# Kernel optimization log

Hardware: AMD Instinct MI355X
Metric: run time of the kernel (lower is better)

## Reference

```python
import jax, jax.numpy as jnp
import numpy as np

N, E, G = 100000, 400000, 2000   # nodes, edges, graphs
IN, H = 48, 128                  # in_channels, hidden_channels (= out_channels)
L = 6                            # num GIN layers
EPS = 1e-5                       # BatchNorm eps
SLOPE = 0.01                     # leaky_relu negative slope


def setup_inputs() -> dict:
    key = jax.random.key(0)
    ks = jax.random.split(key, 12)
    x = jax.random.normal(ks[0], (N, IN), jnp.float32)
    edge_index = jax.random.randint(ks[1], (2, E), 0, N)
    edge_attr = jax.random.normal(ks[2], (E, 4), jnp.float32)  # ignored by GINConv
    # sorted graph-assignment vector; guarantee every graph has >=1 node
    batch = jnp.sort(jnp.concatenate([jnp.arange(G),
                                      jax.random.randint(ks[3], (N - G,), 0, G)]))
    s = 0.05
    W1a = jax.random.normal(ks[4], (IN, H), jnp.float32) * s        # layer-0 MLP lin1
    W1b = jax.random.normal(ks[5], (L - 1, H, H), jnp.float32) * s  # layers 1..5 MLP lin1
    b1 = jnp.zeros((L, H), jnp.float32)
    g1 = jnp.ones((L, H), jnp.float32)    # inner BN scale
    be1 = jnp.zeros((L, H), jnp.float32)  # inner BN bias
    W2 = jax.random.normal(ks[6], (L, H, H), jnp.float32) * s       # MLP lin2
    b2 = jnp.zeros((L, H), jnp.float32)
    gn = jnp.ones((L - 1, H), jnp.float32)    # outer BN scale (layers 0..4)
    bn_b = jnp.zeros((L - 1, H), jnp.float32) # outer BN bias
    fc_w = jax.random.normal(ks[7], (2 * H, 64), jnp.float32) * s
    fc_b = jnp.zeros((64,), jnp.float32)
    fc2_w = jax.random.normal(ks[8], (64, 3), jnp.float32) * s
    fc2_b = jnp.zeros((3,), jnp.float32)
    return dict(x=x, edge_attr=edge_attr, W1a=W1a, W1b=W1b, b1=b1, g1=g1, be1=be1,
                W2=W2, b2=b2, gn=gn, bn_b=bn_b, fc_w=fc_w, fc_b=fc_b,
                fc2_w=fc2_w, fc2_b=fc2_b, edge_index=edge_index, batch=batch,
                num_graphs=G)


def _bn(h, g, b):
    # training-mode BatchNorm1d over node dim (biased variance, as torch)
    m = jnp.mean(h, axis=0)
    v = jnp.mean((h - m) ** 2, axis=0)
    return g * (h - m) * jax.lax.rsqrt(v + EPS) + b


def _lrelu(h):
    return jnp.where(h >= 0, h, SLOPE * h)


def reference(x, edge_attr, W1a, W1b, b1, g1, be1, W2, b2, gn, bn_b,
              fc_w, fc_b, fc2_w, fc2_b, edge_index, batch, num_graphs):
    del edge_attr  # GINConv does not use edge attributes
    src, dst = edge_index[0], edge_index[1]
    n = x.shape[0]
    h = x
    for l in range(L):
        # GINConv: (1 + eps) * x + sum_{j in N(i)} x_j, eps = 0
        agg = jax.ops.segment_sum(h[src], dst, num_segments=n)
        z = h + agg
        W1 = W1a if l == 0 else W1b[l - 1]
        # MLP([in, H, H]) with inner BatchNorm + leaky_relu, plain last linear
        z = _lrelu(_bn(z @ W1 + b1[l], g1[l], be1[l])) @ W2[l] + b2[l]
        if l < L - 1:  # outer norm + act, skipped on last layer
            z = _lrelu(_bn(z, gn[l], bn_b[l]))
        h = z
    # dual global pooling over ragged per-graph segments
    cnt = jax.ops.segment_sum(jnp.ones((n, 1), h.dtype), batch, num_segments=num_graphs)
    p1 = jax.ops.segment_sum(h, batch, num_segments=num_graphs) / jnp.maximum(cnt, 1.0)
    p2 = jax.ops.segment_max(h, batch, num_segments=num_graphs)
    emb = jnp.concatenate([p1, p2], axis=1)            # [G, 256]
    out = _lrelu(emb @ fc_w + fc_b) @ fc2_w + fc2_b    # [G, 3]
    return out, emb
```

## Files before the change

### kernel.cpp

```cpp
#include <hip/hip_runtime.h>
#include <stdint.h>

#define N_NODES 100000
#define N_EDGES 400000
#define N_GRAPHS 2000
#define C_IN 48
#define HD 128
#define NLAYERS 6
#define BN_EPS 1e-5f
#define NSLOPE 0.01f
#define SB 391
#define NREP 8
#define DBINS 33

typedef uint16_t u16;
typedef uint32_t u32;
typedef short bf16x8 __attribute__((ext_vector_type(8)));
typedef float f32x4 __attribute__((ext_vector_type(4)));

__device__ __forceinline__ float bf2f_lo(u32 v) { return __uint_as_float(v << 16); }
__device__ __forceinline__ float bf2f_hi(u32 v) { return __uint_as_float(v & 0xffff0000u); }
__device__ __forceinline__ float bf2f(u16 h) { return __uint_as_float(((u32)h) << 16); }
__device__ __forceinline__ u16 f2bf(float f) {
    u32 u = __float_as_uint(f);
    u32 r = (u + 0x7fffu + ((u >> 16) & 1u)) >> 16;
    return (u16)r;
}
__device__ __forceinline__ u32 pack2(float a, float b) {
    return (u32)f2bf(a) | ((u32)f2bf(b) << 16);
}
__device__ __forceinline__ float lrelu(float v) { return v >= 0.f ? v : v * NSLOPE; }

__device__ __forceinline__ void acc_bn(float* a, const uint4 v, const float* cA, const float* cB) {
    const u32 w[4] = {v.x, v.y, v.z, v.w};
    #pragma unroll
    for (int p = 0; p < 4; ++p) {
        a[2 * p]     += lrelu(cA[2 * p] * bf2f_lo(w[p]) + cB[2 * p]);
        a[2 * p + 1] += lrelu(cA[2 * p + 1] * bf2f_hi(w[p]) + cB[2 * p + 1]);
    }
}
__device__ __forceinline__ void acc_bf16row(float* a, const uint4 v) {
    const u32 w[4] = {v.x, v.y, v.z, v.w};
    #pragma unroll
    for (int p = 0; p < 4; ++p) {
        a[2 * p]     += bf2f_lo(w[p]);
        a[2 * p + 1] += bf2f_hi(w[p]);
    }
}
__device__ __forceinline__ void acc_f32row(float* a, const float* p) {
    const float4 u0 = reinterpret_cast<const float4*>(p)[0];
    const float4 u1 = reinterpret_cast<const float4*>(p)[1];
    a[0] += u0.x; a[1] += u0.y; a[2] += u0.z; a[3] += u0.w;
    a[4] += u1.x; a[5] += u1.y; a[6] += u1.z; a[7] += u1.w;
}
__device__ __forceinline__ void ld_xrow(float* a, const void* xv, int md, int idx, int seg) {
    if (md) acc_f32row(a, (const float*)xv + (size_t)idx * C_IN + seg * 8);
    else    acc_bf16row(a, *reinterpret_cast<const uint4*>((const u16*)xv + (size_t)idx * C_IN + seg * 8));
}

__global__ __launch_bounds__(256) void detect_kernel(const u16* __restrict__ x, int* __restrict__ mode) {
    __shared__ int flag;
    if (threadIdx.x == 0) flag = 0;
    __syncthreads();
    int local = 0;
    for (int i = threadIdx.x; i < 16384; i += 256) {
        float a = fabsf(bf2f(x[i]));
        if (!(a < 1e4f)) local = 1;
    }
    if (local) flag = 1;
    __syncthreads();
    if (threadIdx.x == 0) mode[0] = flag;
}

__global__ __launch_bounds__(256) void hist_kernel(const int* __restrict__ dst, int* __restrict__ cnt) {
    int e = blockIdx.x * 256 + threadIdx.x;
    if (e < N_EDGES) atomicAdd(&cnt[dst[e]], 1);
}

__global__ __launch_bounds__(256) void scan1_kernel(const int* __restrict__ cnt, int* __restrict__ bsum) {
    __shared__ int s[256];
    const int t = threadIdx.x;
    const int i = blockIdx.x * 256 + t;
    s[t] = (i < N_NODES) ? cnt[i] : 0;
    __syncthreads();
    for (int d = 128; d > 0; d >>= 1) {
        if (t < d) s[t] += s[t + d];
        __syncthreads();
    }
    if (t == 0) bsum[blockIdx.x] = s[0];
}

__global__ __launch_bounds__(512) void scan2_kernel(int* __restrict__ bsum, int* __restrict__ row_ptr) {
    __shared__ int s[SB];
    const int t = threadIdx.x;
    if (t < SB) s[t] = bsum[t];
    __syncthreads();
    if (t == 0) {
        int run = 0;
        for (int b = 0; b < SB; ++b) { int v = s[b]; s[b] = run; run += v; }
        row_ptr[0] = 0;
    }
    __syncthreads();
    if (t < SB) bsum[t] = s[t];
}

__global__ __launch_bounds__(256) void scan3_kernel(const int* __restrict__ cnt, const int* __restrict__ bsum,
                                                    int* __restrict__ row_ptr) {
    __shared__ int s[256];
    const int t = threadIdx.x;
    const int i = blockIdx.x * 256 + t;
    s[t] = (i < N_NODES) ? cnt[i] : 0;
    __syncthreads();
    if (t == 0) {
        int run = bsum[blockIdx.x];
        for (int j = 0; j < 256; ++j) { run += s[j]; s[j] = run; }
    }
    __syncthreads();
    if (i < N_NODES) row_ptr[i + 1] = s[t];
}

__global__ __launch_bounds__(256) void fill_kernel(const int* __restrict__ src, const int* __restrict__ dst,
                                                   const int* __restrict__ pos,
                                                   int* __restrict__ cursor, int* __restrict__ col_idx) {
    int e = blockIdx.x * 256 + threadIdx.x;
    if (e < N_EDGES) {
        int d = dst[e];
        int slot = atomicAdd(&cursor[d], 1);
        col_idx[slot] = pos[src[e]];
    }
}

__global__ __launch_bounds__(256) void deg_hist_kernel(const int* __restrict__ row_ptr, int* __restrict__ dbins) {
    __shared__ int h[DBINS];
    const int tid = threadIdx.x;
    if (tid < DBINS) h[tid] = 0;
    __syncthreads();
    const int i = blockIdx.x * 256 + tid;
    if (i < N_NODES) atomicAdd(&h[min(row_ptr[i + 1] - row_ptr[i], 32)], 1);
    __syncthreads();
    if (tid < DBINS && h[tid]) atomicAdd(&dbins[tid], h[tid]);
}

__global__ __launch_bounds__(64) void deg_scan_kernel(int* __restrict__ dbins) {
    if (threadIdx.x == 0) {
        int run = 0;
        for (int b = DBINS - 1; b >= 0; --b) { int v = dbins[b]; dbins[b] = run; run += v; }
    }
}

__global__ __launch_bounds__(256) void deg_scatter_kernel(const int* __restrict__ row_ptr, int* __restrict__ dbins,
                                                          int* __restrict__ perm) {
    __shared__ int cnt[DBINS];
    __shared__ int base[DBINS];
    const int tid = threadIdx.x;
    const int i = blockIdx.x * 256 + tid;
    if (tid < DBINS) cnt[tid] = 0;
    __syncthreads();
    int d = 0, local = 0;
    const bool act = i < N_NODES;
    if (act) {
        d = min(row_ptr[i + 1] - row_ptr[i], 32);
        local = atomicAdd(&cnt[d], 1);
    }
    __syncthreads();
    if (tid < DBINS) base[tid] = cnt[tid] ? atomicAdd(&dbins[tid], cnt[tid]) : 0;
    __syncthreads();
    if (act) perm[base[d] + local] = i;
}

__global__ __launch_bounds__(256) void inv_kernel(const int* __restrict__ perm, int* __restrict__ pos) {
    const int i = blockIdx.x * 256 + threadIdx.x;
    if (i < N_NODES) pos[perm[i]] = i;
}

__global__ __launch_bounds__(256) void pack_w_kernel(const void* __restrict__ W1a, const void* __restrict__ W1b,
                                                     const void* __restrict__ W2, const int* __restrict__ mode,
                                                     u16* __restrict__ wpack) {
    const int t = blockIdx.x * 256 + threadIdx.x;
    if (t >= 24576) return;
    const int mat = t >> 11;
    const int r = t & 2047;
    const int l = r & 63;
    const int f = r >> 6;
    const int kb = f >> 3, nt = f & 7;
    const int k0 = kb * 32 + (l >> 4) * 8;
    const int n = nt * 16 + (l & 15);
    const int md = *mode;
    u16 vals[8];
    #pragma unroll
    for (int j = 0; j < 8; ++j) {
        const int k = k0 + j;
        float v;
        if (mat == 0) {
            v = (k < C_IN) ? (md ? ((const float*)W1a)[k * HD + n] : bf2f(((const u16*)W1a)[k * HD + n])) : 0.f;
        } else if (mat < 6) {
            const size_t o = (size_t)(mat - 1) * HD * HD + (size_t)k * HD + n;
            v = md ? ((const float*)W1b)[o] : bf2f(((const u16*)W1b)[o]);
        } else {
            const size_t o = (size_t)(mat - 6) * HD * HD + (size_t)k * HD + n;
            v = md ? ((const float*)W2)[o] : bf2f(((const u16*)W2)[o]);
        }
        vals[j] = f2bf(v);
    }
    uint4 o;
    o.x = (u32)vals[0] | ((u32)vals[1] << 16);
    o.y = (u32)vals[2] | ((u32)vals[3] << 16);
    o.z = (u32)vals[4] | ((u32)vals[5] << 16);
    o.w = (u32)vals[6] | ((u32)vals[7] << 16);
    *reinterpret_cast<uint4*>(wpack + (size_t)t * 8) = o;
}

__global__ __launch_bounds__(256) void pack_b_kernel(const void* __restrict__ b1, const void* __restrict__ b2,
                                                     const int* __restrict__ mode, float* __restrict__ biasf) {
    const int i = blockIdx.x * 256 + threadIdx.x;
    if (i >= 12 * HD) return;
    const int mat = i >> 7, c = i & 127;
    const int md = *mode;
    float v;
    if (mat < 6) v = md ? ((const float*)b1)[mat * HD + c] : bf2f(((const u16*)b1)[mat * HD + c]);
    else         v = md ? ((const float*)b2)[(mat - 6) * HD + c] : bf2f(((const u16*)b2)[(mat - 6) * HD + c]);
    biasf[i] = v;
}

__device__ __forceinline__ void coef_to_lds(float* coefs, const float* __restrict__ instats,
                                            const void* __restrict__ gammav, const void* __restrict__ betav,
                                            size_t gelem, int md, int tid) {
    if (tid < 128) {
        float sm = 0.f, sq = 0.f;
        #pragma unroll
        for (int rep = 0; rep < NREP; ++rep) {
            sm += instats[rep * 256 + tid];
            sq += instats[rep * 256 + 128 + tid];
        }
        const float inv_n = 1.0f / (float)N_NODES;
        const float mean = sm * inv_n;
        const float var = fmaxf(sq * inv_n - mean * mean, 0.f);
        const float rs = rsqrtf(var + BN_EPS);
        const float g  = md ? ((const float*)gammav)[gelem + tid] : bf2f(((const u16*)gammav)[gelem + tid]);
        const float be = md ? ((const float*)betav)[gelem + tid]  : bf2f(((const u16*)betav)[gelem + tid]);
        const float A = g * rs;
        coefs[tid] = A;
        coefs[128 + tid] = be - A * mean;
    }
}

template <int TRANS, int STATS>
__global__ __launch_bounds__(256) void gemm_mfma(const u16* A, const u16* __restrict__ wp,
                                                 const float* __restrict__ biasf,
                                                 const float* __restrict__ instats,
                                                 const void* __restrict__ gammav, const void* __restrict__ betav,
                                                 size_t gelem, const int* __restrict__ mode,
                                                 u16* out, float* __restrict__ stats) {
    __shared__ u16 Asm[32][136];
    __shared__ float sred[2][128];
    __shared__ float sqred[2][128];
    __shared__ float coefs[256];
    const int tid = threadIdx.x;
    const int m0 = blockIdx.x * 32;
    const int rrow = tid >> 4;
    const int seg = tid & 15;

    if (TRANS) {
        coef_to_lds(coefs, instats, gammav, betav, gelem, *mode, tid);
        __syncthreads();
    }

    {
        float cA[8], cB[8];
        if (TRANS) {
            #pragma unroll
            for (int j = 0; j < 8; ++j) {
                cA[j] = coefs[seg * 8 + j];
                cB[j] = coefs[128 + seg * 8 + j];
            }
        }
        uint4 v[2];
        #pragma unroll
        for (int i = 0; i < 2; ++i) {
            const int gm = m0 + i * 16 + rrow;
            if (gm < N_NODES) v[i] = *reinterpret_cast<const uint4*>(A + (size_t)gm * HD + seg * 8);
            else { v[i].x = 0; v[i].y = 0; v[i].z = 0; v[i].w = 0; }
        }
        #pragma unroll
        for (int i = 0; i < 2; ++i) {
            uint4 o = v[i];
            if (TRANS) {
                u32 w[4] = {o.x, o.y, o.z, o.w};
                #pragma unroll
                for (int p = 0; p < 4; ++p) {
                    const float lo = lrelu(cA[2 * p] * bf2f_lo(w[p]) + cB[2 * p]);
                    const float hi = lrelu(cA[2 * p + 1] * bf2f_hi(w[p]) + cB[2 * p + 1]);
                    w[p] = pack2(lo, hi);
                }
                o.x = w[0]; o.y = w[1]; o.z = w[2]; o.w = w[3];
            }
            *reinterpret_cast<uint4*>(&Asm[i * 16 + rrow][seg * 8]) = o;
        }
    }
    __syncthreads();

    const int wave = tid >> 6, lane = tid & 63;
    const int quad = lane >> 4, lx = lane & 15;
    const int rowhalf = wave & 1;
    const int colhalf = wave >> 1;
    const int wrow = rowhalf * 16;
    f32x4 acc[4] = {};
    #pragma unroll
    for (int kb = 0; kb < 4; ++kb) {
        bf16x8 bfr[4];
        #pragma unroll
        for (int nt = 0; nt < 4; ++nt)
            bfr[nt] = *reinterpret_cast<const bf16x8*>(wp + (((size_t)(kb * 8 + colhalf * 4 + nt) * 64 + lane) << 3));
        const bf16x8 af = *reinterpret_cast<const bf16x8*>(&Asm[wrow + lx][kb * 32 + quad * 8]);
        #pragma unroll
        for (int nt = 0; nt < 4; ++nt)
            acc[nt] = __builtin_amdgcn_mfma_f32_16x16x32_bf16(af, bfr[nt], acc[nt], 0, 0, 0);
    }

    const int mrow0 = m0 + wrow;
    #pragma unroll
    for (int nt = 0; nt < 4; ++nt) {
        const int n = colhalf * 64 + nt * 16 + lx;
        const float bj = biasf[n];
        float s = 0.f, q = 0.f;
        #pragma unroll
        for (int r = 0; r < 4; ++r) {
            const int m = mrow0 + quad * 4 + r;
            if (m < N_NODES) {
                const float v = acc[nt][r] + bj;
                out[(size_t)m * HD + n] = f2bf(v);
                if (STATS) { s += v; q += v * v; }
            }
        }
        if (STATS) {
            s += __shfl_xor(s, 16); s += __shfl_xor(s, 32);
            q += __shfl_xor(q, 16); q += __shfl_xor(q, 32);
            if (quad == 0) { sred[rowhalf][n] = s; sqred[rowhalf][n] = q; }
        }
    }
    if (STATS) {
        __syncthreads();
        float* sdst = stats + (size_t)(blockIdx.x & (NREP - 1)) * 256;
        if (tid < 128) {
            atomicAdd(&sdst[tid], sred[0][tid] + sred[1][tid]);
        } else if (tid < 256) {
            const int c2 = tid - 128;
            atomicAdd(&sdst[128 + c2], sqred[0][c2] + sqred[1][c2]);
        }
    }
}

__global__ __launch_bounds__(256) void gemm_gather(const u16* __restrict__ U, const int* __restrict__ row_ptr,
                                                   const int* __restrict__ col2, const int* __restrict__ perm,
                                                   const u16* __restrict__ wp,
                                                   const float* __restrict__ biasf,
                                                   const float* __restrict__ instats,
                                                   const void* __restrict__ gammav, const void* __restrict__ betav,
                                                   size_t gelem, const int* __restrict__ mode,
                                                   u16* __restrict__ out, float* __restrict__ stats) {
    __shared__ u16 Asm[32][136];
    __shared__ float sred[2][128];
    __shared__ float sqred[2][128];
    __shared__ float coefs[256];
    const int tid = threadIdx.x;
    const int m0 = blockIdx.x * 32;
    const int rrow = tid >> 4;
    const int seg = tid & 15;

    coef_to_lds(coefs, instats, gammav, betav, gelem, *mode, tid);
    __syncthreads();

    {
        float cA[8], cB[8];
        #pragma unroll
        for (int j = 0; j < 8; ++j) {
            cA[j] = coefs[seg * 8 + j];
            cB[j] = coefs[128 + seg * 8 + j];
        }
        const int lm0 = m0 + rrow;
        const int lm1 = m0 + 16 + rrow;
        const int gm0 = perm[lm0];
        const int gm1 = perm[lm1];
        float a0[8], a1[8];
        #pragma unroll
        for (int j = 0; j < 8; ++j) { a0[j] = 0.f; a1[j] = 0.f; }
        const uint4 v0 = *reinterpret_cast<const uint4*>(U + (size_t)lm0 * HD + seg * 8);
        const uint4 v1 = *reinterpret_cast<const uint4*>(U + (size_t)lm1 * HD + seg * 8);
        acc_bn(a0, v0, cA, cB);
        acc_bn(a1, v1, cA, cB);
        const int s0 = row_ptr[gm0], d0 = row_ptr[gm0 + 1] - s0;
        const int s1 = row_ptr[gm1], d1 = row_ptr[gm1 + 1] - s1;
        const int dm = max(d0, d1);
        for (int t = 0; t < dm; t += 2) {
            const bool p00 = t < d0, p01 = (t + 1) < d0;
            const bool p10 = t < d1, p11 = (t + 1) < d1;
            int i00 = 0, i01 = 0, i10 = 0, i11 = 0;
            if (p00) i00 = col2[s0 + t];
            if (p01) i01 = col2[s0 + t + 1];
            if (p10) i10 = col2[s1 + t];
            if (p11) i11 = col2[s1 + t + 1];
            uint4 r00{}, r01{}, r10{}, r11{};
            if (p00) r00 = *reinterpret_cast<const uint4*>(U + (size_t)i00 * HD + seg * 8);
            if (p01) r01 = *reinterpret_cast<const uint4*>(U + (size_t)i01 * HD + seg * 8);
            if (p10) r10 = *reinterpret_cast<const uint4*>(U + (size_t)i10 * HD + seg * 8);
            if (p11) r11 = *reinterpret_cast<const uint4*>(U + (size_t)i11 * HD + seg * 8);
            if (p00) acc_bn(a0, r00, cA, cB);
            if (p01) acc_bn(a0, r01, cA, cB);
            if (p10) acc_bn(a1, r10, cA, cB);
            if (p11) acc_bn(a1, r11, cA, cB);
        }
        uint4 o0, o1;
        o0.x = pack2(a0[0], a0[1]); o0.y = pack2(a0[2], a0[3]);
        o0.z = pack2(a0[4], a0[5]); o0.w = pack2(a0[6], a0[7]);
        o1.x = pack2(a1[0], a1[1]); o1.y = pack2(a1[2], a1[3]);
        o1.z = pack2(a1[4], a1[5]); o1.w = pack2(a1[6], a1[7]);
        *reinterpret_cast<uint4*>(&Asm[rrow][seg * 8]) = o0;
        *reinterpret_cast<uint4*>(&Asm[16 + rrow][seg * 8]) = o1;
    }
    __syncthreads();

    const int wave = tid >> 6, lane = tid & 63;
    const int quad = lane >> 4, lx = lane & 15;
    const int rowhalf = wave & 1;
    const int colhalf = wave >> 1;
    const int wrow = rowhalf * 16;
    f32x4 acc[4] = {};
    #pragma unroll
    for (int kb = 0; kb < 4; ++kb) {
        bf16x8 bfr[4];
        #pragma unroll
        for (int nt = 0; nt < 4; ++nt)
            bfr[nt] = *reinterpret_cast<const bf16x8*>(wp + (((size_t)(kb * 8 + colhalf * 4 + nt) * 64 + lane) << 3));
        const bf16x8 af = *reinterpret_cast<const bf16x8*>(&Asm[wrow + lx][kb * 32 + quad * 8]);
        #pragma unroll
        for (int nt = 0; nt < 4; ++nt)
            acc[nt] = __builtin_amdgcn_mfma_f32_16x16x32_bf16(af, bfr[nt], acc[nt], 0, 0, 0);
    }

    const int mrow0 = m0 + wrow;
    #pragma unroll
    for (int nt = 0; nt < 4; ++nt) {
        const int n = colhalf * 64 + nt * 16 + lx;
        const float bj = biasf[n];
        float s = 0.f, q = 0.f;
        #pragma unroll
        for (int r = 0; r < 4; ++r) {
            const int m = mrow0 + quad * 4 + r;
            const float v = acc[nt][r] + bj;
            out[(size_t)m * HD + n] = f2bf(v);
            s += v; q += v * v;
        }
        s += __shfl_xor(s, 16); s += __shfl_xor(s, 32);
        q += __shfl_xor(q, 16); q += __shfl_xor(q, 32);
        if (quad == 0) { sred[rowhalf][n] = s; sqred[rowhalf][n] = q; }
    }
    __syncthreads();
    float* sdst = stats + (size_t)(blockIdx.x & (NREP - 1)) * 256;
    if (tid < 128) {
        atomicAdd(&sdst[tid], sred[0][tid] + sred[1][tid]);
    } else if (tid < 256) {
        const int c2 = tid - 128;
        atomicAdd(&sdst[128 + c2], sqred[0][c2] + sqred[1][c2]);
    }
}

__global__ __launch_bounds__(256) void gemm_gather0(const void* __restrict__ xv, const int* __restrict__ row_ptr,
                                                    const int* __restrict__ col2, const int* __restrict__ perm,
                                                    const u16* __restrict__ wp,
                                                    const float* __restrict__ biasf, const int* __restrict__ mode,
                                                    u16* __restrict__ out, float* __restrict__ stats) {
    __shared__ u16 Asm[32][136];
    __shared__ float sred[2][128];
    __shared__ float sqred[2][128];
    const int tid = threadIdx.x;
    const int m0 = blockIdx.x * 32;
    const int rrow = tid >> 4;
    const int seg = tid & 15;
    const int md = *mode;
    const bool act = seg < 6;

    {
        const int lm0 = m0 + rrow;
        const int lm1 = m0 + 16 + rrow;
        const int gm0 = perm[lm0];
        const int gm1 = perm[lm1];
        float a0[8], a1[8];
        #pragma unroll
        for (int j = 0; j < 8; ++j) { a0[j] = 0.f; a1[j] = 0.f; }
        const int s0 = row_ptr[gm0], d0 = row_ptr[gm0 + 1] - s0;
        const int s1 = row_ptr[gm1], d1 = row_ptr[gm1 + 1] - s1;
        if (act) {
            ld_xrow(a0, xv, md, gm0, seg);
            ld_xrow(a1, xv, md, gm1, seg);
            const int dm = max(d0, d1);
            for (int t = 0; t < dm; t += 2) {
                const bool p00 = t < d0, p01 = (t + 1) < d0;
                const bool p10 = t < d1, p11 = (t + 1) < d1;
                int i00 = 0, i01 = 0, i10 = 0, i11 = 0;
                if (p00) i00 = perm[col2[s0 + t]];
                if (p01) i01 = perm[col2[s0 + t + 1]];
                if (p10) i10 = perm[col2[s1 + t]];
                if (p11) i11 = perm[col2[s1 + t + 1]];
                if (p00) ld_xrow(a0, xv, md, i00, seg);
                if (p01) ld_xrow(a0, xv, md, i01, seg);
                if (p10) ld_xrow(a1, xv, md, i10, seg);
                if (p11) ld_xrow(a1, xv, md, i11, seg);
            }
        }
        uint4 o0, o1;
        o0.x = pack2(a0[0], a0[1]); o0.y = pack2(a0[2], a0[3]);
        o0.z = pack2(a0[4], a0[5]); o0.w = pack2(a0[6], a0[7]);
        o1.x = pack2(a1[0], a1[1]); o1.y = pack2(a1[2], a1[3]);
        o1.z = pack2(a1[4], a1[5]); o1.w = pack2(a1[6], a1[7]);
        *reinterpret_cast<uint4*>(&Asm[rrow][seg * 8]) = o0;
        *reinterpret_cast<uint4*>(&Asm[16 + rrow][seg * 8]) = o1;
    }
    __syncthreads();

    const int wave = tid >> 6, lane = tid & 63;
    const int quad = lane >> 4, lx = lane & 15;
    const int rowhalf = wave & 1;
    const int colhalf = wave >> 1;
    const int wrow = rowhalf * 16;
    f32x4 acc[4] = {};
    #pragma unroll
    for (int kb = 0; kb < 4; ++kb) {
        bf16x8 bfr[4];
        #pragma unroll
        for (int nt = 0; nt < 4; ++nt)
            bfr[nt] = *reinterpret_cast<const bf16x8*>(wp + (((size_t)(kb * 8 + colhalf * 4 + nt) * 64 + lane) << 3));
        const bf16x8 af = *reinterpret_cast<const bf16x8*>(&Asm[wrow + lx][kb * 32 + quad * 8]);
        #pragma unroll
        for (int nt = 0; nt < 4; ++nt)
            acc[nt] = __builtin_amdgcn_mfma_f32_16x16x32_bf16(af, bfr[nt], acc[nt], 0, 0, 0);
    }

    const int mrow0 = m0 + wrow;
    #pragma unroll
    for (int nt = 0; nt < 4; ++nt) {
        const int n = colhalf * 64 + nt * 16 + lx;
        const float bj = biasf[n];
        float s = 0.f, q = 0.f;
        #pragma unroll
        for (int r = 0; r < 4; ++r) {
            const int m = mrow0 + quad * 4 + r;
            const float v = acc[nt][r] + bj;
            out[(size_t)m * HD + n] = f2bf(v);
            s += v; q += v * v;
        }
        s += __shfl_xor(s, 16); s += __shfl_xor(s, 32);
        q += __shfl_xor(q, 16); q += __shfl_xor(q, 32);
        if (quad == 0) { sred[rowhalf][n] = s; sqred[rowhalf][n] = q; }
    }
    __syncthreads();
    float* sdst = stats + (size_t)(blockIdx.x & (NREP - 1)) * 256;
    if (tid < 128) {
        atomicAdd(&sdst[tid], sred[0][tid] + sred[1][tid]);
    } else if (tid < 256) {
        const int c2 = tid - 128;
        atomicAdd(&sdst[128 + c2], sqred[0][c2] + sqred[1][c2]);
    }
}

__global__ __launch_bounds__(256) void pool_kernel(const u16* __restrict__ hf, const int* __restrict__ batch,
                                                   const int* __restrict__ pos,
                                                   const int* __restrict__ mode, float* __restrict__ emb,
                                                   void* __restrict__ outv) {
    const int wave = threadIdx.x >> 6, lane = threadIdx.x & 63;
    const int g = blockIdx.x * 4 + wave;
    if (g >= N_GRAPHS) return;
    const int md = *mode;
    const int quad = lane >> 4, c = lane & 15;
    int lo = 0, hi = N_NODES;
    while (lo < hi) { int m = (lo + hi) >> 1; if (batch[m] < g) lo = m + 1; else hi = m; }
    const int s = lo;
    hi = N_NODES;
    while (lo < hi) { int m = (lo + hi) >> 1; if (batch[m] < g + 1) lo = m + 1; else hi = m; }
    const int e = lo;
    const int cnt = e - s;
    float sum[8], mx[8];
    #pragma unroll
    for (int j = 0; j < 8; ++j) { sum[j] = 0.f; mx[j] = -INFINITY; }
    for (int n = s + quad; n < e; n += 4) {
        const int p = pos[n];
        const uint4 v = *reinterpret_cast<const uint4*>(hf + (size_t)p * HD + c * 8);
        const u32 w[4] = {v.x, v.y, v.z, v.w};
        #pragma unroll
        for (int pp = 0; pp < 4; ++pp) {
            const float f0 = bf2f_lo(w[pp]), f1 = bf2f_hi(w[pp]);
            sum[2 * pp] += f0; sum[2 * pp + 1] += f1;
            mx[2 * pp] = fmaxf(mx[2 * pp], f0); mx[2 * pp + 1] = fmaxf(mx[2 * pp + 1], f1);
        }
    }
    #pragma unroll
    for (int j = 0; j < 8; ++j) {
        sum[j] += __shfl_xor(sum[j], 16); sum[j] += __shfl_xor(sum[j], 32);
        mx[j] = fmaxf(mx[j], __shfl_xor(mx[j], 16));
        mx[j] = fmaxf(mx[j], __shfl_xor(mx[j], 32));
    }
    if (quad == 0) {
        const float invc = 1.0f / (float)max(cnt, 1);
        const size_t base = (size_t)N_GRAPHS * 3 + (size_t)g * 256;
        #pragma unroll
        for (int j = 0; j < 8; ++j) {
            const float mean = sum[j] * invc;
            const float m2 = (cnt == 0) ? 0.f : mx[j];
            const int col = c * 8 + j;
            emb[(size_t)g * 256 + col] = mean;
            emb[(size_t)g * 256 + 128 + col] = m2;
            if (md) {
                ((float*)outv)[base + col] = mean;
                ((float*)outv)[base + 128 + col] = m2;
            } else {
                ((u16*)outv)[base + col] = f2bf(mean);
                ((u16*)outv)[base + 128 + col] = f2bf(m2);
            }
        }
    }
}

__global__ __launch_bounds__(64) void final_kernel(const float* __restrict__ emb, const void* __restrict__ fcwv,
                                                   const void* __restrict__ fcbv, const void* __restrict__ fc2wv,
                                                   const void* __restrict__ fc2bv, const int* __restrict__ mode,
                                                   void* __restrict__ outv) {
    __shared__ float es[256];
    __shared__ float hs[64];
    const int g = blockIdx.x, t = threadIdx.x;
    const int md = *mode;
    reinterpret_cast<float4*>(es)[t] = reinterpret_cast<const float4*>(emb + (size_t)g * 256)[t];
    __syncthreads();
    float acc = md ? ((const float*)fcbv)[t] : bf2f(((const u16*)fcbv)[t]);
    if (md) {
        const float* w = (const float*)fcwv;
        #pragma unroll 8
        for (int k = 0; k < 256; ++k) acc += es[k] * w[k * 64 + t];
    } else {
        const u16* w = (const u16*)fcwv;
        #pragma unroll 8
        for (int k = 0; k < 256; ++k) acc += es[k] * bf2f(w[k * 64 + t]);
    }
    hs[t] = lrelu(acc);
    __syncthreads();
    if (t < 3) {
        float o = md ? ((const float*)fc2bv)[t] : bf2f(((const u16*)fc2bv)[t]);
        if (md) {
            const float* w = (const float*)fc2wv;
            #pragma unroll 8
            for (int j = 0; j < 64; ++j) o += hs[j] * w[j * 3 + t];
            ((float*)outv)[(size_t)g * 3 + t] = o;
        } else {
            const u16* w = (const u16*)fc2wv;
            #pragma unroll 8
            for (int j = 0; j < 64; ++j) o += hs[j] * bf2f(w[j * 3 + t]);
            ((u16*)outv)[(size_t)g * 3 + t] = f2bf(o);
        }
    }
}

static inline size_t align256(size_t x) { return (x + 255) & ~(size_t)255; }

extern "C" void kernel_launch(void* const* d_in, const int* in_sizes, int n_in,
                              void* d_out, int out_size, void* d_ws, size_t ws_size,
                              hipStream_t stream) {
    (void)in_sizes; (void)n_in; (void)out_size; (void)ws_size;
    const void* x    = d_in[0];
    const void* W1a  = d_in[2];
    const void* W1b  = d_in[3];
    const void* b1   = d_in[4];
    const void* g1   = d_in[5];
    const void* be1  = d_in[6];
    const void* W2   = d_in[7];
    const void* b2   = d_in[8];
    const void* gn   = d_in[9];
    const void* bnb  = d_in[10];
    const void* fcw  = d_in[11];
    const void* fcb  = d_in[12];
    const void* fc2w = d_in[13];
    const void* fc2b = d_in[14];
    const int* ei    = (const int*)d_in[15];
    const int* batch = (const int*)d_in[16];

    char* p = (char*)d_ws;
    size_t off = 0;
    u16* zb = (u16*)(p + off); off += align256((size_t)N_NODES * HD * 2);
    u16* hb = (u16*)(p + off); off += align256((size_t)N_NODES * HD * 2);
    u16* wpack = (u16*)(p + off); off += align256((size_t)12 * HD * HD * 2);
    float* biasf = (float*)(p + off); off += align256((size_t)12 * HD * 4);
    float* emb = (float*)(p + off); off += align256((size_t)N_GRAPHS * 256 * 4);
    int* row_ptr = (int*)(p + off); off += align256((size_t)(N_NODES + 1) * 4);
    int* cursor = (int*)(p + off); off += align256((size_t)N_NODES * 4);
    int* col_idx = (int*)(p + off); off += align256((size_t)N_EDGES * 4);
    int* bsum = (int*)(p + off); off += align256((size_t)SB * 4);
    float* statsAll = (float*)(p + off); off += align256((size_t)12 * NREP * 256 * 4);
    int* perm = (int*)(p + off); off += align256((size_t)N_NODES * 4);
    int* pos = (int*)(p + off); off += align256((size_t)N_NODES * 4);
    int* dbins = (int*)(p + off); off += align256((size_t)64 * 4);
    int* mode = (int*)(p + off); off += align256(4);

    const int EB = (N_EDGES + 255) / 256;
    const int GB32 = N_NODES / 32;

    detect_kernel<<<1, 256, 0, stream>>>((const u16*)x, mode);

    hipMemsetAsync(cursor, 0, (size_t)N_NODES * 4, stream);
    hipMemsetAsync(statsAll, 0, (size_t)12 * NREP * 256 * 4, stream);
    hipMemsetAsync(dbins, 0, (size_t)DBINS * 4, stream);
    hist_kernel<<<EB, 256, 0, stream>>>(ei + N_EDGES, cursor);
    scan1_kernel<<<SB, 256, 0, stream>>>(cursor, bsum);
    scan2_kernel<<<1, 512, 0, stream>>>(bsum, row_ptr);
    scan3_kernel<<<SB, 256, 0, stream>>>(cursor, bsum, row_ptr);
    deg_hist_kernel<<<SB, 256, 0, stream>>>(row_ptr, dbins);
    deg_scan_kernel<<<1, 64, 0, stream>>>(dbins);
    deg_scatter_kernel<<<SB, 256, 0, stream>>>(row_ptr, dbins, perm);
    inv_kernel<<<SB, 256, 0, stream>>>(perm, pos);
    hipMemcpyAsync(cursor, row_ptr, (size_t)N_NODES * 4, hipMemcpyDeviceToDevice, stream);
    fill_kernel<<<EB, 256, 0, stream>>>(ei, ei + N_EDGES, pos, cursor, col_idx);
    pack_w_kernel<<<96, 256, 0, stream>>>(W1a, W1b, W2, mode, wpack);
    pack_b_kernel<<<6, 256, 0, stream>>>(b1, b2, mode, biasf);

    u16* cur = zb;
    u16* oth = hb;
    for (int l = 0; l < NLAYERS; ++l) {
        float* statsA = statsAll + (size_t)l * NREP * 256;
        float* statsB = statsAll + (size_t)(6 + l) * NREP * 256;
        float* statsBprev = statsAll + (size_t)(6 + l - 1) * NREP * 256;
        if (l == 0) {
            gemm_gather0<<<GB32, 256, 0, stream>>>(x, row_ptr, col_idx, perm, wpack,
                                                   biasf, mode, cur, statsA);
        } else {
            gemm_gather<<<GB32, 256, 0, stream>>>(cur, row_ptr, col_idx, perm,
                                                  wpack + (size_t)l * HD * HD,
                                                  biasf + (size_t)l * HD, statsBprev, gn, bnb,
                                                  (size_t)(l - 1) * HD, mode, oth, statsA);
            u16* t = cur; cur = oth; oth = t;
        }
        if (l < NLAYERS - 1) {
            gemm_mfma<1, 1><<<GB32, 256, 0, stream>>>(cur, wpack + (size_t)(6 + l) * HD * HD,
                                                      biasf + (size_t)(6 + l) * HD, statsA, g1, be1,
                                                      (size_t)l * HD, mode, cur, statsB);
        } else {
            gemm_mfma<1, 0><<<GB32, 256, 0, stream>>>(cur, wpack + (size_t)(6 + l) * HD * HD,
                                                      biasf + (size_t)(6 + l) * HD, statsA, g1, be1,
                                                      (size_t)l * HD, mode, cur, nullptr);
        }
    }

    pool_kernel<<<(N_GRAPHS + 3) / 4, 256, 0, stream>>>(cur, batch, pos, mode, emb, d_out);
    final_kernel<<<N_GRAPHS, 64, 0, stream>>>(emb, fcw, fcb, fc2w, fc2b, mode, d_out);
}
```

Baseline: 494.7 us.

## Unroll gathers by four, parallelize block scan, store raw source indices

The neighbor-gather loops in both gather GEMM kernels are unrolled from two to four neighbors per step, so more independent row loads are in flight. Layer 0 now reads a second column array holding raw source ids, which removes the perm indirection per edge at the cost of writing another 400K-int array. The serial single-thread scan in scan2 becomes a parallel Hillis-Steele scan. Row-bound checks in the GEMM are dropped (N is divisible by 32), and the shared epilogue is factored into a helper. The wider unroll raises register pressure.

```diff
diff --git a/kernel.cpp b/kernel.cpp
--- a/kernel.cpp
+++ b/kernel.cpp
@@ -91,17 +91,18 @@
 }
 
 __global__ __launch_bounds__(512) void scan2_kernel(int* __restrict__ bsum, int* __restrict__ row_ptr) {
-    __shared__ int s[SB];
+    __shared__ int s[512];
     const int t = threadIdx.x;
-    if (t < SB) s[t] = bsum[t];
-    __syncthreads();
-    if (t == 0) {
-        int run = 0;
-        for (int b = 0; b < SB; ++b) { int v = s[b]; s[b] = run; run += v; }
-        row_ptr[0] = 0;
-    }
-    __syncthreads();
-    if (t < SB) bsum[t] = s[t];
+    s[t] = (t < SB) ? bsum[t] : 0;
+    __syncthreads();
+    for (int d = 1; d < 512; d <<= 1) {
+        const int v = (t >= d) ? s[t - d] : 0;
+        __syncthreads();
+        s[t] += v;
+        __syncthreads();
+    }
+    if (t < SB) bsum[t] = (t == 0) ? 0 : s[t - 1];
+    if (t == 0) row_ptr[0] = 0;
 }
 
 __global__ __launch_bounds__(256) void scan3_kernel(const int* __restrict__ cnt, const int* __restrict__ bsum,
@@ -121,12 +122,15 @@
 
 __global__ __launch_bounds__(256) void fill_kernel(const int* __restrict__ src, const int* __restrict__ dst,
                                                    const int* __restrict__ pos,
-                                                   int* __restrict__ cursor, int* __restrict__ col_idx) {
+                                                   int* __restrict__ cursor, int* __restrict__ col_idx,
+                                                   int* __restrict__ col0_idx) {
     int e = blockIdx.x * 256 + threadIdx.x;
     if (e < N_EDGES) {
         int d = dst[e];
         int slot = atomicAdd(&cursor[d], 1);
-        col_idx[slot] = pos[src[e]];
+        const int sv = src[e];
+        col_idx[slot] = pos[sv];
+        col0_idx[slot] = sv;
     }
 }
 
@@ -244,6 +248,55 @@
     }
 }
 
+__device__ __forceinline__ void mfma_epilogue32(const u16 (*Asm)[136], const u16* __restrict__ wp,
+                                                const float* __restrict__ biasf,
+                                                float sred[2][128], float sqred[2][128],
+                                                int m0, int tid, int bidx,
+                                                u16* __restrict__ out, float* __restrict__ stats) {
+    const int wave = tid >> 6, lane = tid & 63;
+    const int quad = lane >> 4, lx = lane & 15;
+    const int rowhalf = wave & 1;
+    const int colhalf = wave >> 1;
+    const int wrow = rowhalf * 16;
+    f32x4 acc[4] = {};
+    #pragma unroll
+    for (int kb = 0; kb < 4; ++kb) {
+        bf16x8 bfr[4];
+        #pragma unroll
+        for (int nt = 0; nt < 4; ++nt)
+            bfr[nt] = *reinterpret_cast<const bf16x8*>(wp + (((size_t)(kb * 8 + colhalf * 4 + nt) * 64 + lane) << 3));
+        const bf16x8 af = *reinterpret_cast<const bf16x8*>(&Asm[wrow + lx][kb * 32 + quad * 8]);
+        #pragma unroll
+        for (int nt = 0; nt < 4; ++nt)
+            acc[nt] = __builtin_amdgcn_mfma_f32_16x16x32_bf16(af, bfr[nt], acc[nt], 0, 0, 0);
+    }
+    const int mrow0 = m0 + wrow;
+    #pragma unroll
+    for (int nt = 0; nt < 4; ++nt) {
+        const int n = colhalf * 64 + nt * 16 + lx;
+        const float bj = biasf[n];
+        float s = 0.f, q = 0.f;
+        #pragma unroll
+        for (int r = 0; r < 4; ++r) {
+            const int m = mrow0 + quad * 4 + r;
+            const float v = acc[nt][r] + bj;
+            out[(size_t)m * HD + n] = f2bf(v);
+            s += v; q += v * v;
+        }
+        s += __shfl_xor(s, 16); s += __shfl_xor(s, 32);
+        q += __shfl_xor(q, 16); q += __shfl_xor(q, 32);
+        if (quad == 0) { sred[rowhalf][n] = s; sqred[rowhalf][n] = q; }
+    }
+    __syncthreads();
+    float* sdst = stats + (size_t)(bidx & (NREP - 1)) * 256;
+    if (tid < 128) {
+        atomicAdd(&sdst[tid], sred[0][tid] + sred[1][tid]);
+    } else {
+        const int c2 = tid - 128;
+        atomicAdd(&sdst[128 + c2], sqred[0][c2] + sqred[1][c2]);
+    }
+}
+
 template <int TRANS, int STATS>
 __global__ __launch_bounds__(256) void gemm_mfma(const u16* A, const u16* __restrict__ wp,
                                                  const float* __restrict__ biasf,
@@ -278,8 +331,7 @@
         #pragma unroll
         for (int i = 0; i < 2; ++i) {
             const int gm = m0 + i * 16 + rrow;
-            if (gm < N_NODES) v[i] = *reinterpret_cast<const uint4*>(A + (size_t)gm * HD + seg * 8);
-            else { v[i].x = 0; v[i].y = 0; v[i].z = 0; v[i].w = 0; }
+            v[i] = *reinterpret_cast<const uint4*>(A + (size_t)gm * HD + seg * 8);
         }
         #pragma unroll
         for (int i = 0; i < 2; ++i) {
@@ -299,53 +351,36 @@
     }
     __syncthreads();
 
-    const int wave = tid >> 6, lane = tid & 63;
-    const int quad = lane >> 4, lx = lane & 15;
-    const int rowhalf = wave & 1;
-    const int colhalf = wave >> 1;
-    const int wrow = rowhalf * 16;
-    f32x4 acc[4] = {};
-    #pragma unroll
-    for (int kb = 0; kb < 4; ++kb) {
-        bf16x8 bfr[4];
-        #pragma unroll
-        for (int nt = 0; nt < 4; ++nt)
-            bfr[nt] = *reinterpret_cast<const bf16x8*>(wp + (((size_t)(kb * 8 + colhalf * 4 + nt) * 64 + lane) << 3));
-        const bf16x8 af = *reinterpret_cast<const bf16x8*>(&Asm[wrow + lx][kb * 32 + quad * 8]);
-        #pragma unroll
-        for (int nt = 0; nt < 4; ++nt)
-            acc[nt] = __builtin_amdgcn_mfma_f32_16x16x32_bf16(af, bfr[nt], acc[nt], 0, 0, 0);
-    }
-
-    const int mrow0 = m0 + wrow;
-    #pragma unroll
-    for (int nt = 0; nt < 4; ++nt) {
-        const int n = colhalf * 64 + nt * 16 + lx;
-        const float bj = biasf[n];
-        float s = 0.f, q = 0.f;
-        #pragma unroll
-        for (int r = 0; r < 4; ++r) {
-            const int m = mrow0 + quad * 4 + r;
-            if (m < N_NODES) {
-                const float v = acc[nt][r] + bj;
-                out[(size_t)m * HD + n] = f2bf(v);
-                if (STATS) { s += v; q += v * v; }
+    if (STATS) {
+        mfma_epilogue32(Asm, wp, biasf, sred, sqred, m0, tid, blockIdx.x, out, stats);
+    } else {
+        const int wave = tid >> 6, lane = tid & 63;
+        const int quad = lane >> 4, lx = lane & 15;
+        const int rowhalf = wave & 1;
+        const int colhalf = wave >> 1;
+        const int wrow = rowhalf * 16;
+        f32x4 acc[4] = {};
+        #pragma unroll
+        for (int kb = 0; kb < 4; ++kb) {
+            bf16x8 bfr[4];
+            #pragma unroll
+            for (int nt = 0; nt < 4; ++nt)
+                bfr[nt] = *reinterpret_cast<const bf16x8*>(wp + (((size_t)(kb * 8 + colhalf * 4 + nt) * 64 + lane) << 3));
+            const bf16x8 af = *reinterpret_cast<const bf16x8*>(&Asm[wrow + lx][kb * 32 + quad * 8]);
+            #pragma unroll
+            for (int nt = 0; nt < 4; ++nt)
+                acc[nt] = __builtin_amdgcn_mfma_f32_16x16x32_bf16(af, bfr[nt], acc[nt], 0, 0, 0);
+        }
+        const int mrow0 = m0 + wrow;
+        #pragma unroll
+        for (int nt = 0; nt < 4; ++nt) {
+            const int n = colhalf * 64 + nt * 16 + lx;
+            const float bj = biasf[n];
+            #pragma unroll
+            for (int r = 0; r < 4; ++r) {
+                const int m = mrow0 + quad * 4 + r;
+                out[(size_t)m * HD + n] = f2bf(acc[nt][r] + bj);
             }
-        }
-        if (STATS) {
-            s += __shfl_xor(s, 16); s += __shfl_xor(s, 32);
-            q += __shfl_xor(q, 16); q += __shfl_xor(q, 32);
-            if (quad == 0) { sred[rowhalf][n] = s; sqred[rowhalf][n] = q; }
-        }
-    }
-    if (STATS) {
-        __syncthreads();
-        float* sdst = stats + (size_t)(blockIdx.x & (NREP - 1)) * 256;
-        if (tid < 128) {
-            atomicAdd(&sdst[tid], sred[0][tid] + sred[1][tid]);
-        } else if (tid < 256) {
-            const int c2 = tid - 128;
-            atomicAdd(&sdst[128 + c2], sqred[0][c2] + sqred[1][c2]);
         }
     }
 }
@@ -391,23 +426,36 @@
         const int s0 = row_ptr[gm0], d0 = row_ptr[gm0 + 1] - s0;
         const int s1 = row_ptr[gm1], d1 = row_ptr[gm1 + 1] - s1;
         const int dm = max(d0, d1);
-        for (int t = 0; t < dm; t += 2) {
-            const bool p00 = t < d0, p01 = (t + 1) < d0;
-            const bool p10 = t < d1, p11 = (t + 1) < d1;
-            int i00 = 0, i01 = 0, i10 = 0, i11 = 0;
+        for (int t = 0; t < dm; t += 4) {
+            const bool p00 = t < d0, p01 = (t + 1) < d0, p02 = (t + 2) < d0, p03 = (t + 3) < d0;
+            const bool p10 = t < d1, p11 = (t + 1) < d1, p12 = (t + 2) < d1, p13 = (t + 3) < d1;
+            int i00 = 0, i01 = 0, i02 = 0, i03 = 0;
+            int i10 = 0, i11 = 0, i12 = 0, i13 = 0;
             if (p00) i00 = col2[s0 + t];
             if (p01) i01 = col2[s0 + t + 1];
+            if (p02) i02 = col2[s0 + t + 2];
+            if (p03) i03 = col2[s0 + t + 3];
             if (p10) i10 = col2[s1 + t];
             if (p11) i11 = col2[s1 + t + 1];
-            uint4 r00{}, r01{}, r10{}, r11{};
+            if (p12) i12 = col2[s1 + t + 2];
+            if (p13) i13 = col2[s1 + t + 3];
+            uint4 r00{}, r01{}, r02{}, r03{}, r10{}, r11{}, r12{}, r13{};
             if (p00) r00 = *reinterpret_cast<const uint4*>(U + (size_t)i00 * HD + seg * 8);
             if (p01) r01 = *reinterpret_cast<const uint4*>(U + (size_t)i01 * HD + seg * 8);
+            if (p02) r02 = *reinterpret_cast<const uint4*>(U + (size_t)i02 * HD + seg * 8);
+            if (p03) r03 = *reinterpret_cast<const uint4*>(U + (size_t)i03 * HD + seg * 8);
             if (p10) r10 = *reinterpret_cast<const uint4*>(U + (size_t)i10 * HD + seg * 8);
             if (p11) r11 = *reinterpret_cast<const uint4*>(U + (size_t)i11 * HD + seg * 8);
+            if (p12) r12 = *reinterpret_cast<const uint4*>(U + (size_t)i12 * HD + seg * 8);
+            if (p13) r13 = *reinterpret_cast<const uint4*>(U + (size_t)i13 * HD + seg * 8);
             if (p00) acc_bn(a0, r00, cA, cB);
             if (p01) acc_bn(a0, r01, cA, cB);
+            if (p02) acc_bn(a0, r02, cA, cB);
+            if (p03) acc_bn(a0, r03, cA, cB);
             if (p10) acc_bn(a1, r10, cA, cB);
             if (p11) acc_bn(a1, r11, cA, cB);
+            if (p12) acc_bn(a1, r12, cA, cB);
+            if (p13) acc_bn(a1, r13, cA, cB);
         }
         uint4 o0, o1;
         o0.x = pack2(a0[0], a0[1]); o0.y = pack2(a0[2], a0[3]);
@@ -419,53 +467,11 @@
     }
     __syncthreads();
 
-    const int wave = tid >> 6, lane = tid & 63;
-    const int quad = lane >> 4, lx = lane & 15;
-    const int rowhalf = wave & 1;
-    const int colhalf = wave >> 1;
-    const int wrow = rowhalf * 16;
-    f32x4 acc[4] = {};
-    #pragma unroll
-    for (int kb = 0; kb < 4; ++kb) {
-        bf16x8 bfr[4];
-        #pragma unroll
-        for (int nt = 0; nt < 4; ++nt)
-            bfr[nt] = *reinterpret_cast<const bf16x8*>(wp + (((size_t)(kb * 8 + colhalf * 4 + nt) * 64 + lane) << 3));
-        const bf16x8 af = *reinterpret_cast<const bf16x8*>(&Asm[wrow + lx][kb * 32 + quad * 8]);
-        #pragma unroll
-        for (int nt = 0; nt < 4; ++nt)
-            acc[nt] = __builtin_amdgcn_mfma_f32_16x16x32_bf16(af, bfr[nt], acc[nt], 0, 0, 0);
-    }
-
-    const int mrow0 = m0 + wrow;
-    #pragma unroll
-    for (int nt = 0; nt < 4; ++nt) {
-        const int n = colhalf * 64 + nt * 16 + lx;
-        const float bj = biasf[n];
-        float s = 0.f, q = 0.f;
-        #pragma unroll
-        for (int r = 0; r < 4; ++r) {
-            const int m = mrow0 + quad * 4 + r;
-            const float v = acc[nt][r] + bj;
-            out[(size_t)m * HD + n] = f2bf(v);
-            s += v; q += v * v;
-        }
-        s += __shfl_xor(s, 16); s += __shfl_xor(s, 32);
-        q += __shfl_xor(q, 16); q += __shfl_xor(q, 32);
-        if (quad == 0) { sred[rowhalf][n] = s; sqred[rowhalf][n] = q; }
-    }
-    __syncthreads();
-    float* sdst = stats + (size_t)(blockIdx.x & (NREP - 1)) * 256;
-    if (tid < 128) {
-        atomicAdd(&sdst[tid], sred[0][tid] + sred[1][tid]);
-    } else if (tid < 256) {
-        const int c2 = tid - 128;
-        atomicAdd(&sdst[128 + c2], sqred[0][c2] + sqred[1][c2]);
-    }
+    mfma_epilogue32(Asm, wp, biasf, sred, sqred, m0, tid, blockIdx.x, out, stats);
 }
 
 __global__ __launch_bounds__(256) void gemm_gather0(const void* __restrict__ xv, const int* __restrict__ row_ptr,
-                                                    const int* __restrict__ col2, const int* __restrict__ perm,
+                                                    const int* __restrict__ col0, const int* __restrict__ perm,
                                                     const u16* __restrict__ wp,
                                                     const float* __restrict__ biasf, const int* __restrict__ mode,
                                                     u16* __restrict__ out, float* __restrict__ stats) {
@@ -493,18 +499,27 @@
             ld_xrow(a0, xv, md, gm0, seg);
             ld_xrow(a1, xv, md, gm1, seg);
             const int dm = max(d0, d1);
-            for (int t = 0; t < dm; t += 2) {
-                const bool p00 = t < d0, p01 = (t + 1) < d0;
-                const bool p10 = t < d1, p11 = (t + 1) < d1;
-                int i00 = 0, i01 = 0, i10 = 0, i11 = 0;
-                if (p00) i00 = perm[col2[s0 + t]];
-                if (p01) i01 = perm[col2[s0 + t + 1]];
-                if (p10) i10 = perm[col2[s1 + t]];
-                if (p11) i11 = perm[col2[s1 + t + 1]];
+            for (int t = 0; t < dm; t += 4) {
+                const bool p00 = t < d0, p01 = (t + 1) < d0, p02 = (t + 2) < d0, p03 = (t + 3) < d0;
+                const bool p10 = t < d1, p11 = (t + 1) < d1, p12 = (t + 2) < d1, p13 = (t + 3) < d1;
+                int i00 = 0, i01 = 0, i02 = 0, i03 = 0;
+                int i10 = 0, i11 = 0, i12 = 0, i13 = 0;
+                if (p00) i00 = col0[s0 + t];
+                if (p01) i01 = col0[s0 + t + 1];
+                if (p02) i02 = col0[s0 + t + 2];
+                if (p03) i03 = col0[s0 + t + 3];
+                if (p10) i10 = col0[s1 + t];
+                if (p11) i11 = col0[s1 + t + 1];
+                if (p12) i12 = col0[s1 + t + 2];
+                if (p13) i13 = col0[s1 + t + 3];
                 if (p00) ld_xrow(a0, xv, md, i00, seg);
                 if (p01) ld_xrow(a0, xv, md, i01, seg);
+                if (p02) ld_xrow(a0, xv, md, i02, seg);
+                if (p03) ld_xrow(a0, xv, md, i03, seg);
                 if (p10) ld_xrow(a1, xv, md, i10, seg);
                 if (p11) ld_xrow(a1, xv, md, i11, seg);
+                if (p12) ld_xrow(a1, xv, md, i12, seg);
+                if (p13) ld_xrow(a1, xv, md, i13, seg);
             }
         }
         uint4 o0, o1;
@@ -517,49 +532,7 @@
     }
     __syncthreads();
 
-    const int wave = tid >> 6, lane = tid & 63;
-    const int quad = lane >> 4, lx = lane & 15;
-    const int rowhalf = wave & 1;
-    const int colhalf = wave >> 1;
-    const int wrow = rowhalf * 16;
-    f32x4 acc[4] = {};
-    #pragma unroll
-    for (int kb = 0; kb < 4; ++kb) {
-        bf16x8 bfr[4];
-        #pragma unroll
-        for (int nt = 0; nt < 4; ++nt)
-            bfr[nt] = *reinterpret_cast<const bf16x8*>(wp + (((size_t)(kb * 8 + colhalf * 4 + nt) * 64 + lane) << 3));
-        const bf16x8 af = *reinterpret_cast<const bf16x8*>(&Asm[wrow + lx][kb * 32 + quad * 8]);
-        #pragma unroll
-        for (int nt = 0; nt < 4; ++nt)
-            acc[nt] = __builtin_amdgcn_mfma_f32_16x16x32_bf16(af, bfr[nt], acc[nt], 0, 0, 0);
-    }
-
-    const int mrow0 = m0 + wrow;
-    #pragma unroll
-    for (int nt = 0; nt < 4; ++nt) {
-        const int n = colhalf * 64 + nt * 16 + lx;
-        const float bj = biasf[n];
-        float s = 0.f, q = 0.f;
-        #pragma unroll
-        for (int r = 0; r < 4; ++r) {
-            const int m = mrow0 + quad * 4 + r;
-            const float v = acc[nt][r] + bj;
-            out[(size_t)m * HD + n] = f2bf(v);
-            s += v; q += v * v;
-        }
-        s += __shfl_xor(s, 16); s += __shfl_xor(s, 32);
-        q += __shfl_xor(q, 16); q += __shfl_xor(q, 32);
-        if (quad == 0) { sred[rowhalf][n] = s; sqred[rowhalf][n] = q; }
-    }
-    __syncthreads();
-    float* sdst = stats + (size_t)(blockIdx.x & (NREP - 1)) * 256;
-    if (tid < 128) {
-        atomicAdd(&sdst[tid], sred[0][tid] + sred[1][tid]);
-    } else if (tid < 256) {
-        const int c2 = tid - 128;
-        atomicAdd(&sdst[128 + c2], sqred[0][c2] + sqred[1][c2]);
-    }
+    mfma_epilogue32(Asm, wp, biasf, sred, sqred, m0, tid, blockIdx.x, out, stats);
 }
 
 __global__ __launch_bounds__(256) void pool_kernel(const u16* __restrict__ hf, const int* __restrict__ batch,
@@ -690,6 +663,7 @@
     int* row_ptr = (int*)(p + off); off += align256((size_t)(N_NODES + 1) * 4);
     int* cursor = (int*)(p + off); off += align256((size_t)N_NODES * 4);
     int* col_idx = (int*)(p + off); off += align256((size_t)N_EDGES * 4);
+    int* col0_idx = (int*)(p + off); off += align256((size_t)N_EDGES * 4);
     int* bsum = (int*)(p + off); off += align256((size_t)SB * 4);
     float* statsAll = (float*)(p + off); off += align256((size_t)12 * NREP * 256 * 4);
     int* perm = (int*)(p + off); off += align256((size_t)N_NODES * 4);
@@ -714,7 +688,7 @@
     deg_scatter_kernel<<<SB, 256, 0, stream>>>(row_ptr, dbins, perm);
     inv_kernel<<<SB, 256, 0, stream>>>(perm, pos);
     hipMemcpyAsync(cursor, row_ptr, (size_t)N_NODES * 4, hipMemcpyDeviceToDevice, stream);
-    fill_kernel<<<EB, 256, 0, stream>>>(ei, ei + N_EDGES, pos, cursor, col_idx);
+    fill_kernel<<<EB, 256, 0, stream>>>(ei, ei + N_EDGES, pos, cursor, col_idx, col0_idx);
     pack_w_kernel<<<96, 256, 0, stream>>>(W1a, W1b, W2, mode, wpack);
     pack_b_kernel<<<6, 256, 0, stream>>>(b1, b2, mode, biasf);
 
@@ -725,7 +699,7 @@
         float* statsB = statsAll + (size_t)(6 + l) * NREP * 256;
         float* statsBprev = statsAll + (size_t)(6 + l - 1) * NREP * 256;
         if (l == 0) {
-            gemm_gather0<<<GB32, 256, 0, stream>>>(x, row_ptr, col_idx, perm, wpack,
+            gemm_gather0<<<GB32, 256, 0, stream>>>(x, row_ptr, col0_idx, perm, wpack,
                                                    biasf, mode, cur, statsA);
         } else {
             gemm_gather<<<GB32, 256, 0, stream>>>(cur, row_ptr, col_idx, perm,
```

After: 478.7 us, median of 2. 3.2% less time.
